# Optimization experiments

Hardware: AMD Instinct MI355X
Metric: run time of the kernel (lower is better)

The kernel has to match this reference:

```python
import jax, jax.numpy as jnp
import numpy as np

HIDDEN = 1024
HEADS = 16
HEAD_DIM = HIDDEN // HEADS
SCALE = HEAD_DIM ** (-0.5)


def setup_inputs() -> dict:
    key = jax.random.key(0)
    ks = jax.random.split(key, 5)
    B, N, C = 8, 1024, HIDDEN
    x = jax.random.normal(ks[0], (B, N, C), dtype=jnp.float32)
    # torch nn.Linear params: weight [out, in], bias [out]
    w_in = jax.random.normal(ks[1], (3 * C, C), dtype=jnp.float32) * (C ** -0.5)
    b_in = jax.random.normal(ks[2], (3 * C,), dtype=jnp.float32) * 0.02
    w_out = jax.random.normal(ks[3], (C, C), dtype=jnp.float32) * (C ** -0.5)
    b_out = jax.random.normal(ks[4], (C,), dtype=jnp.float32) * 0.02
    return {"x": x, "w_in": w_in, "b_in": b_in, "w_out": w_out, "b_out": b_out}


def reference(x, w_in, b_in, w_out, b_out):
    B, N, C = x.shape
    H, D = HEADS, HEAD_DIM
    # in_proj: [B,N,3C] -> (3,B,H,N,D)
    qkv = x @ w_in.T + b_in
    qkv = qkv.reshape(B, N, 3, H, D).transpose(2, 0, 3, 1, 4)
    q, k, v = qkv[0], qkv[1], qkv[2]
    # attention scores scaled after QK^T (same math as scaling q)
    attn = jnp.einsum("bhnd,bhmd->bhnm", q, k) * SCALE
    attn = jax.nn.softmax(attn, axis=-1)
    out = jnp.einsum("bhnm,bhmd->bhnd", attn, v)  # [B,H,N,D]
    out = out.transpose(0, 2, 1, 3).reshape(B, N, C)
    return out @ w_out.T + b_out
```

## Files before the change

kernel.cpp:

```cpp
#include <hip/hip_runtime.h>


typedef __attribute__((ext_vector_type(8))) __bf16 bf16x8;
typedef __attribute__((ext_vector_type(4))) __bf16 bf16x4;
typedef __attribute__((ext_vector_type(4))) float f32x4;
typedef __attribute__((ext_vector_type(4))) short short4v;

__device__ __forceinline__ f32x4 mfma16(bf16x8 a, bf16x8 b, f32x4 c) {
  return __builtin_amdgcn_mfma_f32_16x16x32_bf16(a, b, c, 0, 0, 0);
}

#if __has_builtin(__builtin_amdgcn_mfma_f32_16x16x16bf16_1k)
__device__ __forceinline__ f32x4 mfma_pv(bf16x4 a, bf16x4 b, f32x4 c) {
  short4v as = __builtin_bit_cast(short4v, a);
  short4v bs = __builtin_bit_cast(short4v, b);
  return __builtin_amdgcn_mfma_f32_16x16x16bf16_1k(as, bs, c, 0, 0, 0);
}
#else
__device__ __forceinline__ f32x4 mfma_pv(bf16x4 a, bf16x4 b, f32x4 c) {
  __bf16 z = (__bf16)0.f;
  bf16x8 a8 = {a[0], a[1], a[2], a[3], z, z, z, z};
  bf16x8 b8 = {b[0], b[1], b[2], b[3], z, z, z, z};
  return mfma16(a8, b8, c);
}
#endif

__device__ __forceinline__ float fexp2(float x) {
#if __has_builtin(__builtin_amdgcn_exp2f)
  return __builtin_amdgcn_exp2f(x);
#else
  return exp2f(x);
#endif
}

typedef __attribute__((address_space(1))) const unsigned int gu32;
typedef __attribute__((address_space(3))) unsigned int lu32;

__device__ __forceinline__ void async16(const void* g, void* l) {
  __builtin_amdgcn_global_load_lds((gu32*)g, (lu32*)l, 16, 0, 0);
}

__global__ __launch_bounds__(256) void cvt_all(const float* __restrict__ x,
                                               __bf16* __restrict__ xb,
                                               const float* __restrict__ wi,
                                               __bf16* __restrict__ wib,
                                               const float* __restrict__ wo,
                                               __bf16* __restrict__ wob) {
  int blk = blockIdx.x;
  const float* in;
  __bf16* out;
  int base;
  if (blk < 4096)      { in = x;  out = xb;  base = 0; }
  else if (blk < 5632) { in = wi; out = wib; base = 4096; }
  else                 { in = wo; out = wob; base = 5632; }
  int i = ((blk - base) * 256 + threadIdx.x) * 8;
  float4 a = *(const float4*)(in + i);
  float4 b = *(const float4*)(in + i + 4);
  bf16x8 o;
  o[0] = (__bf16)a.x; o[1] = (__bf16)a.y; o[2] = (__bf16)a.z; o[3] = (__bf16)a.w;
  o[4] = (__bf16)b.x; o[5] = (__bf16)b.y; o[6] = (__bf16)b.z; o[7] = (__bf16)b.w;
  *(bf16x8*)(out + i) = o;
}

template <bool WRITE_VT>
__global__ __launch_bounds__(512, 4) void gemm1(const __bf16* __restrict__ A,
                                                const __bf16* __restrict__ Bm,
                                                const float* __restrict__ bias,
                                                __bf16* __restrict__ C,
                                                __bf16* __restrict__ vt) {
  __shared__ char lds[73728];
  const int t = threadIdx.x;
  const int wv = t >> 6, lane = t & 63;
  const int q16 = lane & 15, quad = lane >> 4;
  const int wm = wv >> 1, wn = wv & 1;
  const int bid = blockIdx.x;
  const long m0 = (long)(bid & 31) * 256;
  const long n0 = (long)(bid >> 5) * 128;

  const int sr4 = t >> 2;
  const int gc = (t & 3) ^ ((sr4 >> 2) & 3);
  const int ldst = wv * 1024;

  const __bf16* srcA0 = A + (m0 + sr4) * 1024 + gc * 8;
  const __bf16* srcA1 = A + (m0 + 128 + sr4) * 1024 + gc * 8;
  const __bf16* srcB  = Bm + (n0 + sr4) * 1024 + gc * 8;

  const int raB = (wm * 64 + q16) * 64 + ((quad ^ (q16 >> 2)) * 16);
  const int rbB = (wn * 64 + q16) * 64 + ((quad ^ (q16 >> 2)) * 16);

  f32x4 zero = {0.f, 0.f, 0.f, 0.f};
  f32x4 acc[4][4];
#pragma unroll
  for (int i = 0; i < 4; ++i)
#pragma unroll
    for (int j = 0; j < 4; ++j) acc[i][j] = zero;

  {
    char* b0 = lds;
    async16(srcA0, b0 + ldst);
    async16(srcA1, b0 + 8192 + ldst);
    async16(srcB, b0 + 16384 + ldst);
    char* b1 = lds + 24576;
    async16(srcA0 + 32, b1 + ldst);
    async16(srcA1 + 32, b1 + 8192 + ldst);
    async16(srcB + 32, b1 + 16384 + ldst);
  }
  asm volatile("s_waitcnt vmcnt(3)" ::);
  __builtin_amdgcn_s_barrier();

  int bread = 0;
#pragma unroll 1
  for (int t32 = 0; t32 < 32; ++t32) {
    char* Ac = lds + bread * 24576;
    char* Bc = Ac + 16384;

    if (t32 < 30) {
      int bst = bread + 2;
      if (bst >= 3) bst -= 3;
      char* S = lds + bst * 24576;
      const int kt = (t32 + 2) * 32;
      async16(srcA0 + kt, S + ldst);
      async16(srcA1 + kt, S + 8192 + ldst);
      async16(srcB + kt, S + 16384 + ldst);
    }

    bf16x8 af[4], bfr[4];
#pragma unroll
    for (int mi = 0; mi < 4; ++mi)
      af[mi] = *(const bf16x8*)(Ac + raB + mi * 1024);
#pragma unroll
    for (int nj = 0; nj < 4; ++nj)
      bfr[nj] = *(const bf16x8*)(Bc + rbB + nj * 1024);

    __builtin_amdgcn_s_barrier();
    __builtin_amdgcn_s_setprio(1);
#pragma unroll
    for (int mi = 0; mi < 4; ++mi)
#pragma unroll
      for (int nj = 0; nj < 4; ++nj)
        acc[mi][nj] = mfma16(af[mi], bfr[nj], acc[mi][nj]);
    __builtin_amdgcn_s_setprio(0);

    if (t32 < 30) {
      asm volatile("s_waitcnt vmcnt(3)" ::);
    } else if (t32 == 30) {
      asm volatile("s_waitcnt vmcnt(0)" ::);
    }
    __builtin_amdgcn_s_barrier();
    bread = bread + 1;
    if (bread >= 3) bread -= 3;
  }

  if (WRITE_VT && n0 >= 2048) {
    const int b = (int)(m0 >> 10);
    const int nbase = (int)(m0 & 1023) + wm * 64;
#pragma unroll
    for (int nj = 0; nj < 4; ++nj) {
      int col = (int)n0 + wn * 64 + nj * 16 + q16;
      int cc = col - 2048;
      int h = cc >> 6, d = cc & 63;
      float bs = bias[col];
      __bf16* vrow = vt + (((long)(b * 16 + h)) << 16) + (long)d * 1024;
#pragma unroll
      for (int mi = 0; mi < 4; ++mi) {
        int n = nbase + mi * 16 + quad * 4;
        bf16x4 o;
#pragma unroll
        for (int r = 0; r < 4; ++r) o[r] = (__bf16)(acc[mi][nj][r] + bs);
        *(bf16x4*)(vrow + n) = o;
      }
    }
  } else {
#pragma unroll
    for (int nj = 0; nj < 4; ++nj) {
      long col = n0 + wn * 64 + nj * 16 + q16;
      float bs = bias[col];
#pragma unroll
      for (int mi = 0; mi < 4; ++mi) {
        long rowb = m0 + wm * 64 + mi * 16 + quad * 4;
#pragma unroll
        for (int r = 0; r < 4; ++r) {
          float v = acc[mi][nj][r] + bs;
          C[(rowb + r) * 3072 + col] = (__bf16)v;
        }
      }
    }
  }
}

template <typename OutT>
__global__ __launch_bounds__(256) void gemm_nt64(const __bf16* __restrict__ A,
                                                 const __bf16* __restrict__ Bm,
                                                 const float* __restrict__ bias,
                                                 OutT* __restrict__ C, int K, int ldc) {
  __shared__ __bf16 As[64 * 64];
  __shared__ __bf16 Bs[128 * 64];
  const int t = threadIdx.x;
  const int wv = t >> 6, lane = t & 63;
  const int q16 = lane & 15, quad = lane >> 4;
  const int wm = wv >> 1, wn = wv & 1;
  const long m0 = (long)blockIdx.x * 64;
  const long n0 = (long)blockIdx.y * 128;

  f32x4 zero = {0.f, 0.f, 0.f, 0.f};
  f32x4 acc[2][4];
#pragma unroll
  for (int i = 0; i < 2; ++i)
#pragma unroll
    for (int j = 0; j < 4; ++j) acc[i][j] = zero;

  char* AsB = (char*)As;
  char* BsB = (char*)Bs;
  const int sr = t >> 3;
  const int gc = (t & 7) ^ (sr & 7);

  for (int kt = 0; kt < K; kt += 64) {
    __syncthreads();
#pragma unroll
    for (int i = 0; i < 2; ++i)
      async16(A + (m0 + i * 32 + sr) * K + kt + gc * 8, AsB + i * 4096 + wv * 1024);
#pragma unroll
    for (int i = 0; i < 4; ++i)
      async16(Bm + (n0 + i * 32 + sr) * K + kt + gc * 8, BsB + i * 4096 + wv * 1024);
    __syncthreads();

#pragma unroll
    for (int kk = 0; kk < 2; ++kk) {
      bf16x8 af[2], bf[4];
#pragma unroll
      for (int i = 0; i < 2; ++i) {
        int ra = wm * 32 + i * 16 + q16;
        af[i] = *(const bf16x8*)(AsB + ra * 128 + (((kk * 4 + quad) ^ (ra & 7)) * 16));
      }
#pragma unroll
      for (int j = 0; j < 4; ++j) {
        int rb = wn * 64 + j * 16 + q16;
        bf[j] = *(const bf16x8*)(BsB + rb * 128 + (((kk * 4 + quad) ^ (rb & 7)) * 16));
      }
#pragma unroll
      for (int i = 0; i < 2; ++i)
#pragma unroll
        for (int j = 0; j < 4; ++j) acc[i][j] = mfma16(af[i], bf[j], acc[i][j]);
    }
  }

#pragma unroll
  for (int j = 0; j < 4; ++j) {
    long col = n0 + wn * 64 + j * 16 + q16;
    float bs = bias[col];
#pragma unroll
    for (int i = 0; i < 2; ++i) {
      long rowb = m0 + wm * 32 + i * 16 + quad * 4;
#pragma unroll
      for (int r = 0; r < 4; ++r) {
        float v = acc[i][j][r] + bs;
        C[(rowb + r) * (long)ldc + col] = (OutT)v;
      }
    }
  }
}

__global__ __launch_bounds__(256) void attn_kernel(const __bf16* __restrict__ qkv,
                                                   const __bf16* __restrict__ vt,
                                                   __bf16* __restrict__ ao) {
  __shared__ __bf16 Ks[64 * 64];
  __shared__ __bf16 Vt[64 * 64];
  const int t = threadIdx.x;
  const int wv = t >> 6, lane = t & 63;
  const int q16 = lane & 15, quad = lane >> 4;
  const int bh = blockIdx.x;
  const int b = bh >> 4, h = bh & 15;
  const int q0 = blockIdx.y * 64;
  const long rowbase = (long)b * 1024;

  bf16x8 qf0, qf1;
  {
    long qrow = rowbase + q0 + wv * 16 + q16;
    const __bf16* qp = qkv + qrow * 3072 + h * 64 + quad * 8;
    qf0 = *(const bf16x8*)qp;
    qf1 = *(const bf16x8*)(qp + 32);
#pragma unroll
    for (int j = 0; j < 8; ++j) {
      qf0[j] = (__bf16)((float)qf0[j] * 0.18033688f);
      qf1[j] = (__bf16)((float)qf1[j] * 0.18033688f);
    }
  }

  f32x4 zero = {0.f, 0.f, 0.f, 0.f};
  f32x4 oacc[4];
#pragma unroll
  for (int dt = 0; dt < 4; ++dt) oacc[dt] = zero;
  float lcol = 0.f;

  char* KsB = (char*)Ks;
  char* VtB = (char*)Vt;
  const int sr = t >> 3;
  const int sgc = (t & 7) ^ (sr & 7);
  const int sw = q16 & 7;

  for (int kv0 = 0; kv0 < 1024; kv0 += 64) {
    __syncthreads();
    const __bf16* kg = qkv + (rowbase + kv0 + sr) * 3072 + 1024 + h * 64 + sgc * 8;
    async16(kg, KsB + wv * 1024);
    async16(kg + (long)32 * 3072, KsB + 4096 + wv * 1024);
    const __bf16* vg = vt + (long)bh * 65536 + (long)sr * 1024 + kv0 + sgc * 8;
    async16(vg, VtB + wv * 1024);
    async16(vg + (long)32 * 1024, VtB + 4096 + wv * 1024);
    __syncthreads();

    f32x4 sacc[4];
#pragma unroll
    for (int nt = 0; nt < 4; ++nt) sacc[nt] = zero;
#pragma unroll
    for (int nt = 0; nt < 4; ++nt) {
      int kvr = nt * 16 + q16;
      bf16x8 kf0 = *(const bf16x8*)(KsB + kvr * 128 + ((quad ^ sw) * 16));
      bf16x8 kf1 = *(const bf16x8*)(KsB + kvr * 128 + (((4 + quad) ^ sw) * 16));
      sacc[nt] = mfma16(kf0, qf0, sacc[nt]);
      sacc[nt] = mfma16(kf1, qf1, sacc[nt]);
    }

    bf16x4 pf[4];
#pragma unroll
    for (int nt = 0; nt < 4; ++nt)
#pragma unroll
      for (int r = 0; r < 4; ++r) {
        float p = fexp2(sacc[nt][r]);
        lcol += p;
        pf[nt][r] = (__bf16)p;
      }

#pragma unroll
    for (int nt = 0; nt < 4; ++nt) {
      int c = ((nt * 2 + (quad >> 1)) ^ sw) * 16 + (quad & 1) * 8;
#pragma unroll
      for (int dt = 0; dt < 4; ++dt) {
        bf16x4 vf = *(const bf16x4*)(VtB + (dt * 16 + q16) * 128 + c);
        oacc[dt] = mfma_pv(pf[nt], vf, oacc[dt]);
      }
    }
  }

  lcol += __shfl_xor(lcol, 16);
  lcol += __shfl_xor(lcol, 32);
  float inv = 1.0f / lcol;
#pragma unroll
  for (int r = 0; r < 4; ++r) {
    float ir = __shfl(inv, quad * 4 + r);
    long orow = rowbase + q0 + wv * 16 + quad * 4 + r;
#pragma unroll
    for (int dt = 0; dt < 4; ++dt)
      ao[orow * 1024 + h * 64 + dt * 16 + q16] = (__bf16)(oacc[dt][r] * ir);
  }
}

extern "C" void kernel_launch(void* const* d_in, const int* in_sizes, int n_in,
                              void* d_out, int out_size, void* d_ws, size_t ws_size,
                              hipStream_t stream) {
  const float* x     = (const float*)d_in[0];
  const float* w_in  = (const float*)d_in[1];
  const float* b_in  = (const float*)d_in[2];
  const float* w_out = (const float*)d_in[3];
  const float* b_out = (const float*)d_in[4];
  float* out = (float*)d_out;

  char* ws = (char*)d_ws;
  __bf16* xb   = (__bf16*)(ws);
  __bf16* wib  = (__bf16*)(ws + 16777216);
  __bf16* wob  = (__bf16*)(ws + 23068672);
  __bf16* qkvb = (__bf16*)(ws + 25165824);
  __bf16* aob  = (__bf16*)(ws + 75497472);
  __bf16* vtg  = (__bf16*)d_out;

  cvt_all<<<6144, 256, 0, stream>>>(x, xb, w_in, wib, w_out, wob);
  gemm1<true><<<768, 512, 0, stream>>>(xb, wib, b_in, qkvb, vtg);
  attn_kernel<<<dim3(128, 16), 256, 0, stream>>>(qkvb, vtg, aob);
  gemm_nt64<float><<<dim3(128, 8), 256, 0, stream>>>(
      aob, wob, b_out, out, 1024, 1024);
}
```

Measured before the change: 234.7 us.

## Switch gemm1 to double-buffered LDS pipeline with new swizzle

Reduces the QKV GEMM's LDS ring from three stages to two (48KB), prefetching one k-tile ahead and synchronizing with __syncthreads each iteration instead of explicit vmcnt waits plus two barriers. The launch-bounds occupancy hint is raised from 4 to 6 and the LDS XOR swizzle pattern is changed to use bits 1-2 of the row. The aim is higher occupancy and simpler synchronization, at the cost of a shallower prefetch that exposes more global-load latency. There is also a correctness risk: __syncthreads may not drain the async global-to-LDS loads before the next tile is read.

```diff
diff --git a/kernel.cpp b/kernel.cpp
--- a/kernel.cpp
+++ b/kernel.cpp
@@ -63,12 +63,12 @@
 }
 
 template <bool WRITE_VT>
-__global__ __launch_bounds__(512, 4) void gemm1(const __bf16* __restrict__ A,
+__global__ __launch_bounds__(512, 6) void gemm1(const __bf16* __restrict__ A,
                                                 const __bf16* __restrict__ Bm,
                                                 const float* __restrict__ bias,
                                                 __bf16* __restrict__ C,
                                                 __bf16* __restrict__ vt) {
-  __shared__ char lds[73728];
+  __shared__ char lds[49152];
   const int t = threadIdx.x;
   const int wv = t >> 6, lane = t & 63;
   const int q16 = lane & 15, quad = lane >> 4;
@@ -78,15 +78,15 @@
   const long n0 = (long)(bid >> 5) * 128;
 
   const int sr4 = t >> 2;
-  const int gc = (t & 3) ^ ((sr4 >> 2) & 3);
+  const int gc = (t & 3) ^ ((sr4 >> 1) & 3);
   const int ldst = wv * 1024;
 
   const __bf16* srcA0 = A + (m0 + sr4) * 1024 + gc * 8;
   const __bf16* srcA1 = A + (m0 + 128 + sr4) * 1024 + gc * 8;
   const __bf16* srcB  = Bm + (n0 + sr4) * 1024 + gc * 8;
 
-  const int raB = (wm * 64 + q16) * 64 + ((quad ^ (q16 >> 2)) * 16);
-  const int rbB = (wn * 64 + q16) * 64 + ((quad ^ (q16 >> 2)) * 16);
+  const int raB = (wm * 64 + q16) * 64 + ((quad ^ ((q16 >> 1) & 3)) * 16);
+  const int rbB = (wn * 64 + q16) * 64 + ((quad ^ ((q16 >> 1) & 3)) * 16);
 
   f32x4 zero = {0.f, 0.f, 0.f, 0.f};
   f32x4 acc[4][4];
@@ -95,30 +95,20 @@
 #pragma unroll
     for (int j = 0; j < 4; ++j) acc[i][j] = zero;
 
-  {
-    char* b0 = lds;
-    async16(srcA0, b0 + ldst);
-    async16(srcA1, b0 + 8192 + ldst);
-    async16(srcB, b0 + 16384 + ldst);
-    char* b1 = lds + 24576;
-    async16(srcA0 + 32, b1 + ldst);
-    async16(srcA1 + 32, b1 + 8192 + ldst);
-    async16(srcB + 32, b1 + 16384 + ldst);
-  }
-  asm volatile("s_waitcnt vmcnt(3)" ::);
-  __builtin_amdgcn_s_barrier();
-
-  int bread = 0;
+  async16(srcA0, lds + ldst);
+  async16(srcA1, lds + 8192 + ldst);
+  async16(srcB, lds + 16384 + ldst);
+  __syncthreads();
+
+  int cur = 0;
 #pragma unroll 1
   for (int t32 = 0; t32 < 32; ++t32) {
-    char* Ac = lds + bread * 24576;
+    char* Ac = lds + cur * 24576;
     char* Bc = Ac + 16384;
 
-    if (t32 < 30) {
-      int bst = bread + 2;
-      if (bst >= 3) bst -= 3;
-      char* S = lds + bst * 24576;
-      const int kt = (t32 + 2) * 32;
+    if (t32 < 31) {
+      char* S = lds + (cur ^ 1) * 24576;
+      const int kt = (t32 + 1) * 32;
       async16(srcA0 + kt, S + ldst);
       async16(srcA1 + kt, S + 8192 + ldst);
       async16(srcB + kt, S + 16384 + ldst);
@@ -132,7 +122,6 @@
     for (int nj = 0; nj < 4; ++nj)
       bfr[nj] = *(const bf16x8*)(Bc + rbB + nj * 1024);
 
-    __builtin_amdgcn_s_barrier();
     __builtin_amdgcn_s_setprio(1);
 #pragma unroll
     for (int mi = 0; mi < 4; ++mi)
@@ -141,14 +130,8 @@
         acc[mi][nj] = mfma16(af[mi], bfr[nj], acc[mi][nj]);
     __builtin_amdgcn_s_setprio(0);
 
-    if (t32 < 30) {
-      asm volatile("s_waitcnt vmcnt(3)" ::);
-    } else if (t32 == 30) {
-      asm volatile("s_waitcnt vmcnt(0)" ::);
-    }
-    __builtin_amdgcn_s_barrier();
-    bread = bread + 1;
-    if (bread >= 3) bread -= 3;
+    __syncthreads();
+    cur ^= 1;
   }
 
   if (WRITE_VT && n0 >= 2048) {
```

Measured after the change: 658.1 us. +180.4%, slower.
